# Optimization experiments

Measured on AMD Instinct MI355X. Metric: run time of the kernel, lower is better.

## Reference

```python
import jax, jax.numpy as jnp
import numpy as np

EPS = 0.5          # residual scaling (module __init__ eps)
N = 100_000        # num nodes
E = 1_250_000      # num edges (avg degree ~12.5)
D = 64             # feature dim


def setup_inputs() -> dict:
    key = jax.random.key(0)
    k1, k2, k3 = jax.random.split(key, 3)
    x = jax.random.normal(k1, (N, D), dtype=jnp.float32)
    src = jax.random.randint(k2, (E,), 0, N, dtype=jnp.int32)
    dst = jax.random.randint(k3, (E,), 0, N, dtype=jnp.int32)
    return {"x": x, "src": src, "dst": dst}


def reference(x, src, dst):
    n = x.shape[0]
    # out-degree of each node = number of edges with that node as source
    deg = jax.ops.segment_sum(jnp.ones(src.shape, dtype=x.dtype), src, num_segments=n)
    norm = jnp.power(jnp.maximum(deg, 1.0), -0.5)          # [N]
    edge_norm = norm[src] * norm[dst]                      # [E] (u_mul_v)
    msg = x[src] * edge_norm[:, None]                      # [E, D] (u_mul_e)
    h = jax.ops.segment_sum(msg, dst, num_segments=n)      # sum per destination
    return h + x * EPS
```

## Files before the change

kernel.cpp:

```cpp
#include <hip/hip_runtime.h>

constexpr int D        = 64;
constexpr float EPS    = 0.5f;
constexpr int BKT      = 128;
constexpr int CAPB_MAX = 2048;
constexpr int EPB      = 4096;
constexpr int NBMAX    = 1024;
constexpr int MAXOVF   = 65536;

__device__ __forceinline__ unsigned int f2bf(float f) {
    unsigned int u = __float_as_uint(f);
    return (u + 0x7FFFu + ((u >> 16) & 1u)) >> 16;
}
__device__ __forceinline__ float bf2f_lo(unsigned int v) { return __uint_as_float(v << 16); }
__device__ __forceinline__ float bf2f_hi(unsigned int v) { return __uint_as_float(v & 0xFFFF0000u); }


__global__ void init_kernel(int* __restrict__ curD, int* __restrict__ curS,
                            int* __restrict__ ovf_cnt, int* __restrict__ sovf_cnt,
                            int NB, int capb) {
    int i = blockIdx.x * blockDim.x + threadIdx.x;
    if (i < NB) { curD[i] = i * capb; curS[i] = i * capb; }
    if (i == 0) { *ovf_cnt = 0; *sovf_cnt = 0; }
}

__global__ __launch_bounds__(256)
void partition_kernel(const int* __restrict__ src, const int* __restrict__ dst,
                      int* __restrict__ curD, int* __restrict__ curS,
                      unsigned int* __restrict__ rec, unsigned char* __restrict__ srec,
                      int* __restrict__ ovf_cnt, int* __restrict__ ovf,
                      int* __restrict__ sovf_cnt, int* __restrict__ sovf,
                      int E, int NB, int capb) {
    __shared__ int histD[NBMAX];
    __shared__ int histS[NBMAX];
    __shared__ int startD[NBMAX];
    __shared__ int startS[NBMAX];
    const int base = blockIdx.x * EPB;
    const int tid  = threadIdx.x;
    for (int b = tid; b < NB; b += 256) { histD[b] = 0; histS[b] = 0; }
    __syncthreads();

    #pragma unroll
    for (int k = 0; k < EPB / 256; ++k) {
        int e = base + tid + k * 256;
        if (e < E) {
            atomicAdd(&histD[dst[e] >> 7], 1);
            atomicAdd(&histS[src[e] >> 7], 1);
        }
    }
    __syncthreads();
    for (int b = tid; b < NB; b += 256) {
        int c = histD[b];
        startD[b] = (c > 0) ? atomicAdd(&curD[b], c) : 0;
        histD[b] = 0;
        int c2 = histS[b];
        startS[b] = (c2 > 0) ? atomicAdd(&curS[b], c2) : 0;
        histS[b] = 0;
    }
    __syncthreads();
    #pragma unroll
    for (int k = 0; k < EPB / 256; ++k) {
        int e = base + tid + k * 256;
        if (e < E) {
            int s = src[e], t = dst[e];
            int bD = t >> 7;
            int r  = atomicAdd(&histD[bD], 1);
            int pD = startD[bD] + r;
            if (pD < (bD + 1) * capb) {
                rec[pD] = ((unsigned int)s << 7) | (unsigned int)(t & (BKT - 1));
            } else {
                int i = atomicAdd(ovf_cnt, 1);
                if (i < MAXOVF) { ovf[2 * i] = s; ovf[2 * i + 1] = t; }
            }
            int bS = s >> 7;
            int r2 = atomicAdd(&histS[bS], 1);
            int pS = startS[bS] + r2;
            if (pS < (bS + 1) * capb) {
                srec[pS] = (unsigned char)(s & (BKT - 1));
            } else {
                int i = atomicAdd(sovf_cnt, 1);
                if (i < MAXOVF) sovf[i] = s;
            }
        }
    }
}

__global__ __launch_bounds__(256)
void combo_kernel(const unsigned int* __restrict__ rec, const unsigned char* __restrict__ srec,
                  const int* __restrict__ curD, const int* __restrict__ curS,
                  int* __restrict__ csr, int* __restrict__ row_start,
                  int* __restrict__ row_cnt, const float2* __restrict__ x2,
                  float* __restrict__ norm, unsigned int* __restrict__ yh,
                  const int* __restrict__ sovf_cnt, const int* __restrict__ sovf,
                  int n, int NB, int capb) {
    __shared__ unsigned int recs[CAPB_MAX];
    __shared__ int srcs[CAPB_MAX];
    __shared__ int hist[BKT];
    __shared__ int scanv[BKT];
    __shared__ int rankb[BKT];
    __shared__ float nrm[BKT];
    const int tid = threadIdx.x;

    if (blockIdx.x >= NB) {
        int b = blockIdx.x - NB;
        int cnt = curS[b] - b * capb;
        if (cnt > capb) cnt = capb;
        if (tid < BKT) hist[tid] = 0;
        __syncthreads();
        for (int i = tid; i < cnt; i += 256)
            atomicAdd(&hist[srec[(size_t)b * capb + i]], 1);
        __syncthreads();
        int oc = *sovf_cnt;
        if (oc > 0) {
            if (oc > MAXOVF) oc = MAXOVF;
            for (int i = tid; i < oc; i += 256) {
                int s = sovf[i];
                if ((s >> 7) == b) atomicAdd(&hist[s & (BKT - 1)], 1);
            }
            __syncthreads();
        }
        if (tid < BKT) {
            int node = b * BKT + tid;
            float nm = rsqrtf(fmaxf((float)hist[tid], 1.0f));
            nrm[tid] = nm;
            if (node < n) norm[node] = nm;
        }
        __syncthreads();
        int nodes = n - b * BKT;
        if (nodes > BKT) nodes = BKT;
        if (nodes < 0) nodes = 0;
        int total = nodes * (D / 2);
        size_t gbase = (size_t)b * BKT * (D / 2);
        for (int i = tid; i < total; i += 256) {
            float2 v = x2[gbase + i];
            float nm = nrm[i >> 5];
            yh[gbase + i] = f2bf(v.x * nm) | (f2bf(v.y * nm) << 16);
        }
        return;
    }

    const int b = blockIdx.x;
    int cnt = curD[b] - b * capb;
    if (cnt > capb) cnt = capb;
    for (int i = tid; i < cnt; i += 256) recs[i] = rec[(size_t)b * capb + i];
    if (tid < BKT) hist[tid] = 0;
    __syncthreads();
    for (int i = tid; i < cnt; i += 256) atomicAdd(&hist[recs[i] & (BKT - 1)], 1);
    __syncthreads();
    if (tid < BKT) scanv[tid] = hist[tid];
    __syncthreads();
    #pragma unroll
    for (int off = 1; off < BKT; off <<= 1) {
        int t = 0;
        if (tid < BKT && tid >= off) t = scanv[tid - off];
        __syncthreads();
        if (tid < BKT) scanv[tid] += t;
        __syncthreads();
    }
    if (tid < BKT) {
        int excl = scanv[tid] - hist[tid];
        rankb[tid] = excl;
        int node = b * BKT + tid;
        if (node < n) {
            row_start[node] = b * capb + excl;
            row_cnt[node]   = hist[tid];
        }
    }
    __syncthreads();
    for (int i = tid; i < cnt; i += 256) {
        unsigned int v = recs[i];
        int pos = atomicAdd(&rankb[v & (BKT - 1)], 1);
        srcs[pos] = (int)(v >> 7);
    }
    __syncthreads();
    for (int i = tid; i < cnt; i += 256) csr[(size_t)b * capb + i] = srcs[i];
}

__global__ __launch_bounds__(256)
void gather8_kernel(const uint4* __restrict__ yr4, const float4* __restrict__ x4,
                    const int* __restrict__ csr, const int* __restrict__ row_start,
                    const int* __restrict__ row_cnt, const float* __restrict__ norm,
                    float4* __restrict__ out4, int n) {
    int wid  = (blockIdx.x * blockDim.x + threadIdx.x) >> 6;
    int lane = threadIdx.x & 63;
    int fl   = lane & 7;
    int node = wid * 8 + (lane >> 3);
    bool valid = node < n;
    int rs  = valid ? row_start[node] : 0;
    int cnt = valid ? row_cnt[node] : 0;
    int m = cnt;
    m = max(m, __shfl_xor(m, 8));
    m = max(m, __shfl_xor(m, 16));
    m = max(m, __shfl_xor(m, 32));
    float a0 = 0.f, a1 = 0.f, a2 = 0.f, a3 = 0.f, a4 = 0.f, a5 = 0.f, a6 = 0.f, a7 = 0.f;
    for (int k = 0; k < m; k += 4) {
        #pragma unroll
        for (int j = 0; j < 4; ++j) {
            int kj = k + j;
            bool take = kj < cnt;
            int s = csr[rs + (take ? kj : 0)];
            s = take ? s : 0;
            uint4 v = yr4[(size_t)s * 8 + fl];
            if (!take) { v.x = 0u; v.y = 0u; v.z = 0u; v.w = 0u; }
            a0 += bf2f_lo(v.x); a1 += bf2f_hi(v.x);
            a2 += bf2f_lo(v.y); a3 += bf2f_hi(v.y);
            a4 += bf2f_lo(v.z); a5 += bf2f_hi(v.z);
            a6 += bf2f_lo(v.w); a7 += bf2f_hi(v.w);
        }
    }
    if (valid) {
        float nt = norm[node];
        size_t base = (size_t)node * 16 + fl * 2;
        float4 xv0 = x4[base], xv1 = x4[base + 1];
        float4 r0, r1;
        r0.x = a0 * nt + EPS * xv0.x;  r0.y = a1 * nt + EPS * xv0.y;
        r0.z = a2 * nt + EPS * xv0.z;  r0.w = a3 * nt + EPS * xv0.w;
        r1.x = a4 * nt + EPS * xv1.x;  r1.y = a5 * nt + EPS * xv1.y;
        r1.z = a6 * nt + EPS * xv1.z;  r1.w = a7 * nt + EPS * xv1.w;
        out4[base] = r0;
        out4[base + 1] = r1;
    }
}

__global__ void cleanup_kernel(const float* __restrict__ x, const float* __restrict__ norm,
                               const int* __restrict__ ovf_cnt, const int* __restrict__ ovf,
                               float* __restrict__ out) {
    int cnt = *ovf_cnt;
    if (cnt > MAXOVF) cnt = MAXOVF;
    long long total = (long long)cnt * D;
    long long stride = (long long)gridDim.x * blockDim.x;
    for (long long i = blockIdx.x * (long long)blockDim.x + threadIdx.x; i < total; i += stride) {
        int e = (int)(i >> 6), d = (int)(i & 63);
        int s = ovf[2 * e], t = ovf[2 * e + 1];
        atomicAdd(&out[(size_t)t * D + d], norm[s] * norm[t] * x[(size_t)s * D + d]);
    }
}


__global__ void fb_hist(const int* __restrict__ src, int* __restrict__ deg, int E) {
    int e = blockIdx.x * blockDim.x + threadIdx.x;
    if (e < E) atomicAdd(&deg[src[e]], 1);
}
__global__ void fb_norm(const int* __restrict__ deg, float* __restrict__ norm, int n) {
    int i = blockIdx.x * blockDim.x + threadIdx.x;
    if (i < n) norm[i] = rsqrtf(fmaxf((float)deg[i], 1.0f));
}
__global__ void fb_init_out(const float4* __restrict__ x, float4* __restrict__ out, int n4) {
    int i = blockIdx.x * blockDim.x + threadIdx.x;
    if (i < n4) {
        float4 v = x[i];
        out[i] = make_float4(v.x * EPS, v.y * EPS, v.z * EPS, v.w * EPS);
    }
}
__global__ void fb_scatter(const float* __restrict__ x, const int* __restrict__ src,
                           const int* __restrict__ dst, const float* __restrict__ norm,
                           float* __restrict__ out, int E) {
    long long tid = (long long)blockIdx.x * blockDim.x + threadIdx.x;
    int e = (int)(tid >> 6), d = (int)(tid & 63);
    if (e < E) {
        int s = src[e], t = dst[e];
        atomicAdd(&out[(size_t)t * D + d], norm[s] * norm[t] * x[(size_t)s * D + d]);
    }
}


extern "C" void kernel_launch(void* const* d_in, const int* in_sizes, int n_in,
                              void* d_out, int out_size, void* d_ws, size_t ws_size,
                              hipStream_t stream) {
    const float* x   = (const float*)d_in[0];
    const int*   src = (const int*)d_in[1];
    const int*   dst = (const int*)d_in[2];
    float* out = (float*)d_out;

    const int ND = in_sizes[0];
    const int E  = in_sizes[1];
    const int n  = ND / D;
    const int NB = (n + BKT - 1) / BKT;
    constexpr int B = 256;

    int capb = 0;
    for (int c : {2048, 1792}) {
        size_t need = (size_t)NB * c * 4
                    + (size_t)NB * c * 4
                    + (size_t)NB * c
                    + ((size_t)(2 * NB + 127) & ~63ull) * 4
                    + (size_t)n * 4 * 3
                    + (size_t)ND * 2
                    + (size_t)(128 + 3 * MAXOVF) * 4;
        if (need <= ws_size) { capb = c; break; }
    }

    if (NB <= NBMAX && capb > 0 && n < (1 << 24)) {
        unsigned int* rec   = (unsigned int*)d_ws;
        int*   csr          = (int*)(rec + (size_t)NB * capb);
        unsigned char* srec = (unsigned char*)(csr + (size_t)NB * capb);
        int*   curD         = (int*)(srec + (((size_t)NB * capb + 3) & ~3ull));
        int*   curS         = curD + NB;
        float* norm         = (float*)(curS + ((NB + 63) & ~63));
        int*   row_start    = (int*)(norm + n);
        int*   row_cnt      = row_start + n;
        unsigned int* yh    = (unsigned int*)(row_cnt + n);
        int*   ovf_cnt      = (int*)(yh + ND / 2);
        int*   sovf_cnt     = ovf_cnt + 64;
        int*   ovf          = sovf_cnt + 64;
        int*   sovf         = ovf + 2 * MAXOVF;

        init_kernel<<<(NB + B - 1) / B, B, 0, stream>>>(curD, curS, ovf_cnt, sovf_cnt, NB, capb);
        partition_kernel<<<(E + EPB - 1) / EPB, B, 0, stream>>>(src, dst, curD, curS, rec, srec,
                                                                ovf_cnt, ovf, sovf_cnt, sovf,
                                                                E, NB, capb);
        combo_kernel<<<2 * NB, B, 0, stream>>>(rec, srec, curD, curS, csr, row_start, row_cnt,
                                               (const float2*)x, norm, yh, sovf_cnt, sovf,
                                               n, NB, capb);
        gather8_kernel<<<(n + 31) / 32, B, 0, stream>>>((const uint4*)yh, (const float4*)x,
                                                        csr, row_start, row_cnt, norm,
                                                        (float4*)out, n);
        cleanup_kernel<<<64, B, 0, stream>>>(x, norm, ovf_cnt, ovf, out);
    } else {
        int*   deg  = (int*)d_ws;
        float* norm = (float*)d_ws + n;
        hipMemsetAsync(deg, 0, (size_t)n * sizeof(int), stream);
        fb_hist<<<(E + B - 1) / B, B, 0, stream>>>(src, deg, E);
        fb_norm<<<(n + B - 1) / B, B, 0, stream>>>(deg, norm, n);
        fb_init_out<<<(ND / 4 + B - 1) / B, B, 0, stream>>>((const float4*)x, (float4*)out, ND / 4);
        long long total = (long long)E * D;
        fb_scatter<<<(int)((total + B - 1) / B), B, 0, stream>>>(x, src, dst, norm, out, E);
    }
}
```

Baseline: 172.3 us.

## Sort destination nodes by degree before gather to balance wavefront work

Adds a degree histogram in the combo kernel plus two new kernels (bin scan and permutation) that order nodes by in-degree. The gather kernel then processes nodes through this permutation, so the 8 nodes sharing a wavefront have similar edge counts and less of the loop is spent masked off. The partition kernel also keeps src/dst in registers between its two passes instead of reloading them, and processes half as many edges per block. The cost is two extra kernel launches, an extra perm array, and an indirect node lookup that scatters row_start and output accesses.

```diff
diff --git a/kernel.cpp b/kernel.cpp
--- a/kernel.cpp
+++ b/kernel.cpp
@@ -4,9 +4,10 @@
 constexpr float EPS    = 0.5f;
 constexpr int BKT      = 128;
 constexpr int CAPB_MAX = 2048;
-constexpr int EPB      = 4096;
+constexpr int EPB      = 2048;
 constexpr int NBMAX    = 1024;
 constexpr int MAXOVF   = 65536;
+constexpr int NBIN     = 64;
 
 __device__ __forceinline__ unsigned int f2bf(float f) {
     unsigned int u = __float_as_uint(f);
@@ -18,9 +19,10 @@
 
 __global__ void init_kernel(int* __restrict__ curD, int* __restrict__ curS,
                             int* __restrict__ ovf_cnt, int* __restrict__ sovf_cnt,
-                            int NB, int capb) {
+                            int* __restrict__ binHist, int NB, int capb) {
     int i = blockIdx.x * blockDim.x + threadIdx.x;
     if (i < NB) { curD[i] = i * capb; curS[i] = i * capb; }
+    if (i < NBIN) binHist[i] = 0;
     if (i == 0) { *ovf_cnt = 0; *sovf_cnt = 0; }
 }
 
@@ -40,12 +42,15 @@
     for (int b = tid; b < NB; b += 256) { histD[b] = 0; histS[b] = 0; }
     __syncthreads();
 
+    int2 ed[EPB / 256];
     #pragma unroll
     for (int k = 0; k < EPB / 256; ++k) {
         int e = base + tid + k * 256;
         if (e < E) {
-            atomicAdd(&histD[dst[e] >> 7], 1);
-            atomicAdd(&histS[src[e] >> 7], 1);
+            int s = src[e], t = dst[e];
+            ed[k] = make_int2(s, t);
+            atomicAdd(&histD[t >> 7], 1);
+            atomicAdd(&histS[s >> 7], 1);
         }
     }
     __syncthreads();
@@ -62,7 +67,7 @@
     for (int k = 0; k < EPB / 256; ++k) {
         int e = base + tid + k * 256;
         if (e < E) {
-            int s = src[e], t = dst[e];
+            int s = ed[k].x, t = ed[k].y;
             int bD = t >> 7;
             int r  = atomicAdd(&histD[bD], 1);
             int pD = startD[bD] + r;
@@ -92,13 +97,14 @@
                   int* __restrict__ row_cnt, const float2* __restrict__ x2,
                   float* __restrict__ norm, unsigned int* __restrict__ yh,
                   const int* __restrict__ sovf_cnt, const int* __restrict__ sovf,
-                  int n, int NB, int capb) {
+                  int* __restrict__ binHist, int n, int NB, int capb) {
     __shared__ unsigned int recs[CAPB_MAX];
     __shared__ int srcs[CAPB_MAX];
     __shared__ int hist[BKT];
     __shared__ int scanv[BKT];
     __shared__ int rankb[BKT];
     __shared__ float nrm[BKT];
+    __shared__ int lbin[NBIN];
     const int tid = threadIdx.x;
 
     if (blockIdx.x >= NB) {
@@ -144,6 +150,7 @@
     if (cnt > capb) cnt = capb;
     for (int i = tid; i < cnt; i += 256) recs[i] = rec[(size_t)b * capb + i];
     if (tid < BKT) hist[tid] = 0;
+    if (tid < NBIN) lbin[tid] = 0;
     __syncthreads();
     for (int i = tid; i < cnt; i += 256) atomicAdd(&hist[recs[i] & (BKT - 1)], 1);
     __syncthreads();
@@ -164,9 +171,11 @@
         if (node < n) {
             row_start[node] = b * capb + excl;
             row_cnt[node]   = hist[tid];
-        }
-    }
-    __syncthreads();
+            atomicAdd(&lbin[min(hist[tid], NBIN - 1)], 1);
+        }
+    }
+    __syncthreads();
+    if (tid < NBIN && lbin[tid] > 0) atomicAdd(&binHist[tid], lbin[tid]);
     for (int i = tid; i < cnt; i += 256) {
         unsigned int v = recs[i];
         int pos = atomicAdd(&rankb[v & (BKT - 1)], 1);
@@ -176,16 +185,57 @@
     for (int i = tid; i < cnt; i += 256) csr[(size_t)b * capb + i] = srcs[i];
 }
 
+__global__ void dscan_kernel(const int* __restrict__ binHist, int* __restrict__ binCursor) {
+    __shared__ int sh[NBIN];
+    int t = threadIdx.x;
+    if (t < NBIN) sh[t] = binHist[t];
+    __syncthreads();
+    if (t == 0) {
+        int run = 0;
+        for (int i = 0; i < NBIN; ++i) { int v = sh[i]; sh[i] = run; run += v; }
+    }
+    __syncthreads();
+    if (t < NBIN) binCursor[t] = sh[t];
+}
+
+__global__ __launch_bounds__(1024)
+void dperm_kernel(const int* __restrict__ row_cnt, int* __restrict__ binCursor,
+                  int* __restrict__ perm, int n) {
+    __shared__ int lhist[NBIN];
+    __shared__ int lstart[NBIN];
+    int tid = threadIdx.x;
+    int node = blockIdx.x * 1024 + tid;
+    if (tid < NBIN) lhist[tid] = 0;
+    __syncthreads();
+    int bin = 0;
+    if (node < n) {
+        bin = min(row_cnt[node], NBIN - 1);
+        atomicAdd(&lhist[bin], 1);
+    }
+    __syncthreads();
+    if (tid < NBIN) {
+        int c = lhist[tid];
+        lstart[tid] = (c > 0) ? atomicAdd(&binCursor[tid], c) : 0;
+        lhist[tid] = 0;
+    }
+    __syncthreads();
+    if (node < n) {
+        int r = atomicAdd(&lhist[bin], 1);
+        perm[lstart[bin] + r] = node;
+    }
+}
+
 __global__ __launch_bounds__(256)
 void gather8_kernel(const uint4* __restrict__ yr4, const float4* __restrict__ x4,
                     const int* __restrict__ csr, const int* __restrict__ row_start,
                     const int* __restrict__ row_cnt, const float* __restrict__ norm,
-                    float4* __restrict__ out4, int n) {
+                    const int* __restrict__ perm, float4* __restrict__ out4, int n) {
     int wid  = (blockIdx.x * blockDim.x + threadIdx.x) >> 6;
     int lane = threadIdx.x & 63;
     int fl   = lane & 7;
-    int node = wid * 8 + (lane >> 3);
-    bool valid = node < n;
+    int slot = wid * 8 + (lane >> 3);
+    bool valid = slot < n;
+    int node = valid ? perm[slot] : 0;
     int rs  = valid ? row_start[node] : 0;
     int cnt = valid ? row_cnt[node] : 0;
     int m = cnt;
@@ -284,9 +334,9 @@
                     + (size_t)NB * c * 4
                     + (size_t)NB * c
                     + ((size_t)(2 * NB + 127) & ~63ull) * 4
-                    + (size_t)n * 4 * 3
+                    + (size_t)n * 4 * 4
                     + (size_t)ND * 2
-                    + (size_t)(128 + 3 * MAXOVF) * 4;
+                    + (size_t)(256 + 3 * MAXOVF) * 4;
         if (need <= ws_size) { capb = c; break; }
     }
 
@@ -299,21 +349,27 @@
         float* norm         = (float*)(curS + ((NB + 63) & ~63));
         int*   row_start    = (int*)(norm + n);
         int*   row_cnt      = row_start + n;
-        unsigned int* yh    = (unsigned int*)(row_cnt + n);
+        int*   perm         = row_cnt + n;
+        unsigned int* yh    = (unsigned int*)(perm + n);
         int*   ovf_cnt      = (int*)(yh + ND / 2);
         int*   sovf_cnt     = ovf_cnt + 64;
-        int*   ovf          = sovf_cnt + 64;
+        int*   binHist      = sovf_cnt + 64;
+        int*   binCursor    = binHist + NBIN;
+        int*   ovf          = binCursor + NBIN;
         int*   sovf         = ovf + 2 * MAXOVF;
 
-        init_kernel<<<(NB + B - 1) / B, B, 0, stream>>>(curD, curS, ovf_cnt, sovf_cnt, NB, capb);
+        init_kernel<<<(NB + B - 1) / B, B, 0, stream>>>(curD, curS, ovf_cnt, sovf_cnt,
+                                                        binHist, NB, capb);
         partition_kernel<<<(E + EPB - 1) / EPB, B, 0, stream>>>(src, dst, curD, curS, rec, srec,
                                                                 ovf_cnt, ovf, sovf_cnt, sovf,
                                                                 E, NB, capb);
         combo_kernel<<<2 * NB, B, 0, stream>>>(rec, srec, curD, curS, csr, row_start, row_cnt,
                                                (const float2*)x, norm, yh, sovf_cnt, sovf,
-                                               n, NB, capb);
+                                               binHist, n, NB, capb);
+        dscan_kernel<<<1, 64, 0, stream>>>(binHist, binCursor);
+        dperm_kernel<<<(n + 1023) / 1024, 1024, 0, stream>>>(row_cnt, binCursor, perm, n);
         gather8_kernel<<<(n + 31) / 32, B, 0, stream>>>((const uint4*)yh, (const float4*)x,
-                                                        csr, row_start, row_cnt, norm,
+                                                        csr, row_start, row_cnt, norm, perm,
                                                         (float4*)out, n);
         cleanup_kernel<<<64, B, 0, stream>>>(x, norm, ovf_cnt, ovf, out);
     } else {
```

Measured after the change: 196.0 us. 1.14x slower.
